# Kernel optimization log

Measured on AMD Instinct MI355X. Metric: run time of the kernel, lower is better.

The kernel has to match this reference:

```python
import jax, jax.numpy as jnp
import numpy as np

B, T, IN, H, NL = 64, 256, 64, 768, 2
LU, OUT = 256, 1
INPUT_SCALE = 1.5
OUTPUT_SCALE = 70.0
STD = 0.001  # nn.init.normal_(p, std=0.001) on all LSTM params


def setup_inputs() -> dict:
    key = jax.random.key(0)
    ks = jax.random.split(key, 16)
    inp = {"x": jax.random.normal(ks[0], (B, T, IN), jnp.float32)}
    dims = [IN, H]
    for l in range(NL):
        d = dims[l]
        inp[f"Wih{l}"] = (jax.random.normal(ks[1 + 4 * l], (4 * H, d)) * STD).astype(jnp.float32)
        inp[f"Whh{l}"] = (jax.random.normal(ks[2 + 4 * l], (4 * H, H)) * STD).astype(jnp.float32)
        inp[f"bih{l}"] = (jax.random.normal(ks[3 + 4 * l], (4 * H,)) * STD).astype(jnp.float32)
        inp[f"bhh{l}"] = (jax.random.normal(ks[4 + 4 * l], (4 * H,)) * STD).astype(jnp.float32)
    # MLP head (torch default-ish small init)
    inp["W1"] = (jax.random.normal(ks[9], (LU, H)) * (1.0 / np.sqrt(H))).astype(jnp.float32)
    inp["b1"] = jnp.zeros((LU,), jnp.float32)
    inp["W2"] = (jax.random.normal(ks[10], (OUT, LU)) * (1.0 / np.sqrt(LU))).astype(jnp.float32)
    inp["b2"] = jnp.zeros((OUT,), jnp.float32)
    return inp


def _lstm_layer(x, Wih, Whh, bih, bhh):
    # x: (B, T, D) -> hidden sequence (B, T, H). PyTorch gate order: i, f, g, o.
    b = x.shape[0]
    h = Whh.shape[1]
    # precompute input contributions for all timesteps: (B, T, 4H)
    xg = jnp.einsum('btd,gd->btg', x, Wih) + bih + bhh

    def step(carry, xt):
        hp, cp = carry
        gates = xt + hp @ Whh.T  # (B, 4H)
        i, f, g, o = jnp.split(gates, 4, axis=-1)
        c = jax.nn.sigmoid(f) * cp + jax.nn.sigmoid(i) * jnp.tanh(g)
        hn = jax.nn.sigmoid(o) * jnp.tanh(c)
        return (hn, c), hn

    h0 = jnp.zeros((b, h), x.dtype)
    (_, _), hs = jax.lax.scan(step, (h0, h0), xg.transpose(1, 0, 2))
    return hs.transpose(1, 0, 2)  # (B, T, H)


def reference(x, Wih0, Whh0, bih0, bhh0, Wih1, Whh1, bih1, bhh1, W1, b1, W2, b2):
    xs = x / INPUT_SCALE
    h1 = _lstm_layer(xs, Wih0, Whh0, bih0, bhh0)
    h2 = _lstm_layer(h1, Wih1, Whh1, bih1, bhh1)
    last = h2[:, -1, :]                       # (B, H)
    z = jax.nn.soft_sign(last @ W1.T + b1)    # Softsign: x / (1 + |x|)
    pred = (z @ W2.T + b2) * OUTPUT_SCALE     # (B, OUT)
    return pred[:, None, :]                   # unsqueeze(1) -> (B, 1, OUT)
```

## Files before the change

kernel.cpp:

```cpp
#include <hip/hip_runtime.h>
#include <hip/hip_bf16.h>


#define B_  64
#define T_  256
#define IN_ 64
#define H_  768
#define G_  3072
#define K0_ 832
#define K1_ 1536
#define NWG0 96
#define NWGC 192
#define NWGT 256
#define CB_  96
#define SLOT_ (CB_ * 64 * 8)

typedef __bf16 bf16_t;
typedef bf16_t bf16x8 __attribute__((ext_vector_type(8)));
typedef float  f32x4  __attribute__((ext_vector_type(4)));

__device__ __forceinline__ unsigned short f2bf(float f) {
    union { float f; unsigned u; } v; v.f = f;
    unsigned r = v.u + 0x7FFFu + ((v.u >> 16) & 1u);
    return (unsigned short)(r >> 16);
}
__device__ __forceinline__ float fast_sigm(float x) {
    float e = __builtin_amdgcn_exp2f(-1.44269504f * x);
    return __builtin_amdgcn_rcpf(1.0f + e);
}
__device__ __forceinline__ float fast_tanh(float x) {
    float e = __builtin_amdgcn_exp2f(2.88539008f * x);
    return (e - 1.0f) * __builtin_amdgcn_rcpf(e + 1.0f);
}
__device__ __forceinline__ void st_llc_u32(unsigned* p, unsigned v) {
    asm volatile("global_store_dword %0, %1, off sc1" :: "v"(p), "v"(v) : "memory");
}
#define MFMA16(a, b, c) __builtin_amdgcn_mfma_f32_16x16x32_bf16((a), (b), (c), 0, 0, 0)
#define AGENT_LD(p) __hip_atomic_load((p), __ATOMIC_RELAXED, __HIP_MEMORY_SCOPE_AGENT)


__global__ __launch_bounds__(256) void prep_kernel(
    const float* __restrict__ x,
    const float* __restrict__ Wih0, const float* __restrict__ Whh0,
    const float* __restrict__ bih0, const float* __restrict__ bhh0,
    const float* __restrict__ Wih1, const float* __restrict__ Whh1,
    const float* __restrict__ bih1, const float* __restrict__ bhh1,
    unsigned short* __restrict__ xsT,
    unsigned short* __restrict__ W0cat,
    unsigned short* __restrict__ W1cat,
    float* __restrict__ bias0, float* __restrict__ bias1,
    int* __restrict__ ctrs)
{
    int i = blockIdx.x * blockDim.x + threadIdx.x;
    int stride = gridDim.x * blockDim.x;
    for (int j = i; j < B_ * T_ * IN_; j += stride) {
        int b = j >> 14;
        int t = (j >> 6) & (T_ - 1);
        int k = j & (IN_ - 1);
        xsT[(((size_t)t * B_) + b) * IN_ + k] = f2bf(x[j] * (1.0f / 1.5f));
    }
    for (int j = i; j < G_ * IN_; j += stride) {
        int r = j >> 6; int k = j & 63;
        W0cat[(size_t)r * K0_ + k] = f2bf(Wih0[j]);
    }
    for (int j = i; j < G_ * H_; j += stride) {
        int r = j / H_; int k = j - r * H_;
        W0cat[(size_t)r * K0_ + IN_ + k] = f2bf(Whh0[j]);
        W1cat[(size_t)r * K1_ + k]       = f2bf(Wih1[j]);
        W1cat[(size_t)r * K1_ + H_ + k]  = f2bf(Whh1[j]);
    }
    for (int j = i; j < G_; j += stride) {
        bias0[j] = bih0[j] + bhh0[j];
        bias1[j] = bih1[j] + bhh1[j];
    }
    for (int j = i; j < 2048; j += stride) ctrs[j] = 0;
}

__global__ __launch_bounds__(256) void lstm_persistent(
    const unsigned short* __restrict__ xsT,
    const unsigned short* __restrict__ W0cat,
    const unsigned short* __restrict__ W1cat,
    const float* __restrict__ bias0, const float* __restrict__ bias1,
    unsigned short* __restrict__ h1ring,
    unsigned short* __restrict__ h2ring,
    float* __restrict__ hf32,
    int* __restrict__ ctrs)
{
    __shared__ unsigned short ldsb[4][16][8];

    const int tid  = threadIdx.x;
    const int lane = tid & 63;
    const int wave = tid >> 6;
    const int wg   = blockIdx.x;

    int* flags0 = &ctrs[0];
    int* flags1 = &ctrs[256];
    int* ep0    = &ctrs[512];
    int* ep1    = &ctrs[768];
    int* done   = &ctrs[1536];

    if (wg == NWGC || wg == NWGC + 1) {
        if (wave != 0) return;
        const bool agg1 = (wg == NWGC + 1);
        int* fl = agg1 ? flags1 : flags0;
        int* ep = agg1 ? ep1 : ep0;
        const int i1 = lane;
        const int i2 = 64 + (lane & 31);
        for (int e = 1; e <= T_; ++e) {
            for (;;) {
                int fa = AGENT_LD(&fl[i1]);
                int fb = AGENT_LD(&fl[i2]);
                if (__all(fa >= e && fb >= e)) break;
                __builtin_amdgcn_s_sleep(1);
            }
            if (lane < 8) st_llc_u32((unsigned*)&ep[lane * 16], (unsigned)e);
        }
        if (agg1 && lane == 0) st_llc_u32((unsigned*)done, 1u);
        return;
    }
    if (wg > NWGC + 1) {
        float a = 1.0f + (float)tid * 1e-7f;
        const float bm = 1.0000001f, cm = 1e-9f;
        for (;;) {
            for (int i = 0; i < 2048; i++)
                a = __builtin_fmaf(a, bm, cm);
            asm volatile("" : "+v"(a));
            int d = 0;
            if (lane == 0) d = AGENT_LD(done);
            d = __builtin_amdgcn_readfirstlane(d);
            if (d != 0) break;
        }
        return;
    }

    const bool isL1 = (wg >= NWG0);
    const int cb   = isL1 ? (wg - NWG0) : wg;
    const int c0   = cb * 8;
    const int frow = lane & 15;
    const int q    = lane >> 4;
    const int kof  = q * 8;
    const int m0   = wave * 16;

    int* myrep0 = &ep0[(wg & 7) * 16];
    int* myrep1 = &ep1[(wg & 7) * 16];

    const unsigned short* Wc = isL1 ? W1cat : W0cat;
    const int Kc = isL1 ? K1_ : K0_;
    int q0 = frow >> 3, col0 = c0 + (frow & 7);
    const unsigned short* Bp0 = Wc + (size_t)(q0 * H_ + col0) * Kc + kof;
    const unsigned short* Bp1 = Wc + (size_t)((2 + q0) * H_ + col0) * Kc + kof;

    const float* bias = isL1 ? bias1 : bias0;
    const bool lowhalf = (lane & 15) < 8;
    const int ecol = c0 + (lane & 7);
    float bi = 0.f, bff = 0.f, bg = 0.f, bo = 0.f;
    if (lowhalf) {
        bi  = bias[0 * H_ + ecol];
        bff = bias[1 * H_ + ecol];
        bg  = bias[2 * H_ + ecol];
        bo  = bias[3 * H_ + ecol];
    }
    float creg[4] = {0.f, 0.f, 0.f, 0.f};

    const size_t aoff = (size_t)q * 512 + (size_t)(m0 + frow) * 8;
    const size_t stoff_e = (size_t)cb * 512 + (size_t)(m0 + (lane >> 2)) * 8
                         + (size_t)(lane & 3) * 2;

    if (!isL1) {
        for (int s = 0; s < T_; ++s) {
            f32x4 acc0 = {0.f, 0.f, 0.f, 0.f};
            f32x4 acc1 = {0.f, 0.f, 0.f, 0.f};
            {
                const unsigned short* xsp =
                    xsT + ((size_t)s * B_ + m0 + frow) * IN_ + kof;
                #pragma unroll
                for (int ki = 0; ki < 2; ki++) {
                    bf16x8 a  = *(const bf16x8*)(xsp + ki * 32);
                    bf16x8 b0 = *(const bf16x8*)(Bp0 + ki * 32);
                    bf16x8 b1 = *(const bf16x8*)(Bp1 + ki * 32);
                    acc0 = MFMA16(a, b0, acc0);
                    acc1 = MFMA16(a, b1, acc1);
                }
            }
            if (s > 0) {
                if (tid == 0) {
                    while (AGENT_LD(myrep0) < s)
                        __builtin_amdgcn_s_sleep(1);
                }
                __syncthreads();
                const unsigned short* hr = h1ring + (size_t)(s - 1) * SLOT_ + aoff;
                #pragma unroll
                for (int kj = 0; kj < 24; kj++) {
                    bf16x8 a  = *(const bf16x8*)(hr + kj * 2048);
                    bf16x8 b0 = *(const bf16x8*)(Bp0 + (kj + 2) * 32);
                    bf16x8 b1 = *(const bf16x8*)(Bp1 + (kj + 2) * 32);
                    acc0 = MFMA16(a, b0, acc0);
                    acc1 = MFMA16(a, b1, acc1);
                }
            }
            f32x4 pacc0, pacc1;
            #pragma unroll
            for (int j = 0; j < 4; j++) {
                pacc0[j] = __shfl_xor(acc0[j], 8);
                pacc1[j] = __shfl_xor(acc1[j], 8);
            }
            if (lowhalf) {
                #pragma unroll
                for (int j = 0; j < 4; j++) {
                    float pi = acc0[j]  + bi;
                    float pf = pacc0[j] + bff;
                    float pg = acc1[j]  + bg;
                    float po = pacc1[j] + bo;
                    float cn = fast_sigm(pf) * creg[j] + fast_sigm(pi) * fast_tanh(pg);
                    float hn = fast_sigm(po) * fast_tanh(cn);
                    creg[j] = cn;
                    ldsb[wave][q * 4 + j][lane & 7] = f2bf(hn);
                }
            }
            unsigned v = ((const unsigned*)&ldsb[wave][0][0])[lane];
            st_llc_u32((unsigned*)(h1ring + (size_t)s * SLOT_ + stoff_e), v);
            __syncthreads();
            if (tid == 0) st_llc_u32((unsigned*)&flags0[cb], (unsigned)(s + 1));
        }
    } else {
        for (int s = 1; s <= T_; ++s) {
            const int t = s - 1;
            if (tid == 0) {
                while (AGENT_LD(myrep0) < s)
                    __builtin_amdgcn_s_sleep(1);
            }
            if (tid == 64 && t > 0) {
                while (AGENT_LD(myrep1) < t)
                    __builtin_amdgcn_s_sleep(1);
            }
            __syncthreads();
            f32x4 acc0 = {0.f, 0.f, 0.f, 0.f};
            f32x4 acc1 = {0.f, 0.f, 0.f, 0.f};
            const unsigned short* h1r = h1ring + (size_t)t * SLOT_ + aoff;
            #pragma unroll
            for (int ki = 0; ki < 24; ki++) {
                bf16x8 a  = *(const bf16x8*)(h1r + ki * 2048);
                bf16x8 b0 = *(const bf16x8*)(Bp0 + ki * 32);
                bf16x8 b1 = *(const bf16x8*)(Bp1 + ki * 32);
                acc0 = MFMA16(a, b0, acc0);
                acc1 = MFMA16(a, b1, acc1);
            }
            if (t > 0) {
                const unsigned short* h2r = h2ring + (size_t)(t - 1) * SLOT_ + aoff;
                #pragma unroll
                for (int ki = 0; ki < 24; ki++) {
                    bf16x8 a  = *(const bf16x8*)(h2r + ki * 2048);
                    bf16x8 b0 = *(const bf16x8*)(Bp0 + (ki + 24) * 32);
                    bf16x8 b1 = *(const bf16x8*)(Bp1 + (ki + 24) * 32);
                    acc0 = MFMA16(a, b0, acc0);
                    acc1 = MFMA16(a, b1, acc1);
                }
            }
            f32x4 pacc0, pacc1;
            #pragma unroll
            for (int j = 0; j < 4; j++) {
                pacc0[j] = __shfl_xor(acc0[j], 8);
                pacc1[j] = __shfl_xor(acc1[j], 8);
            }
            if (lowhalf) {
                #pragma unroll
                for (int j = 0; j < 4; j++) {
                    int row = m0 + q * 4 + j;
                    float pi = acc0[j]  + bi;
                    float pf = pacc0[j] + bff;
                    float pg = acc1[j]  + bg;
                    float po = pacc1[j] + bo;
                    float cn = fast_sigm(pf) * creg[j] + fast_sigm(pi) * fast_tanh(pg);
                    float hn = fast_sigm(po) * fast_tanh(cn);
                    creg[j] = cn;
                    ldsb[wave][q * 4 + j][lane & 7] = f2bf(hn);
                    if (t == T_ - 1) hf32[(size_t)row * H_ + ecol] = hn;
                }
            }
            unsigned v = ((const unsigned*)&ldsb[wave][0][0])[lane];
            st_llc_u32((unsigned*)(h2ring + (size_t)t * SLOT_ + stoff_e), v);
            __syncthreads();
            if (tid == 0) st_llc_u32((unsigned*)&flags1[cb], (unsigned)s);
        }
    }
}

__global__ __launch_bounds__(256) void head_kernel(
    const float* __restrict__ hlast,
    const float* __restrict__ W1, const float* __restrict__ b1,
    const float* __restrict__ W2, const float* __restrict__ b2,
    float* __restrict__ out)
{
    __shared__ float hs[H_];
    __shared__ float partial[4];
    int b = blockIdx.x;
    int tid = threadIdx.x;
    for (int j = tid; j < H_; j += 256) hs[j] = hlast[(size_t)b * H_ + j];
    __syncthreads();
    float z = 0.f;
    const float* w = W1 + (size_t)tid * H_;
    for (int j = 0; j < H_; j++) z += hs[j] * w[j];
    z += b1[tid];
    z = z / (1.0f + fabsf(z));
    float p = z * W2[tid];
    #pragma unroll
    for (int off = 32; off > 0; off >>= 1) p += __shfl_down(p, off, 64);
    if ((tid & 63) == 0) partial[tid >> 6] = p;
    __syncthreads();
    if (tid == 0) {
        float s = partial[0] + partial[1] + partial[2] + partial[3];
        out[b] = (s + b2[0]) * 70.0f;
    }
}

extern "C" void kernel_launch(void* const* d_in, const int* in_sizes, int n_in,
                              void* d_out, int out_size, void* d_ws, size_t ws_size,
                              hipStream_t stream) {
    const float* x    = (const float*)d_in[0];
    const float* Wih0 = (const float*)d_in[1];
    const float* Whh0 = (const float*)d_in[2];
    const float* bih0 = (const float*)d_in[3];
    const float* bhh0 = (const float*)d_in[4];
    const float* Wih1 = (const float*)d_in[5];
    const float* Whh1 = (const float*)d_in[6];
    const float* bih1 = (const float*)d_in[7];
    const float* bhh1 = (const float*)d_in[8];
    const float* W1   = (const float*)d_in[9];
    const float* b1   = (const float*)d_in[10];
    const float* W2   = (const float*)d_in[11];
    const float* b2   = (const float*)d_in[12];
    float* out = (float*)d_out;

    char* w = (char*)d_ws;
    int* ctrs = (int*)w;                          w += 8192;
    unsigned short* h1ring = (unsigned short*)w;  w += (size_t)T_ * SLOT_ * 2;
    unsigned short* h2ring = (unsigned short*)w;  w += (size_t)T_ * SLOT_ * 2;
    unsigned short* xsT    = (unsigned short*)w;  w += (size_t)B_ * T_ * IN_ * 2;
    unsigned short* W0cat  = (unsigned short*)w;  w += (size_t)G_ * K0_ * 2;
    unsigned short* W1cat  = (unsigned short*)w;  w += (size_t)G_ * K1_ * 2;
    float* bias0 = (float*)w;                     w += G_ * 4;
    float* bias1 = (float*)w;                     w += G_ * 4;
    float* hf32  = (float*)w;                     w += (size_t)B_ * H_ * 4;

    prep_kernel<<<1024, 256, 0, stream>>>(x, Wih0, Whh0, bih0, bhh0,
                                          Wih1, Whh1, bih1, bhh1,
                                          xsT, W0cat, W1cat, bias0, bias1, ctrs);
    lstm_persistent<<<NWGT, 256, 0, stream>>>(xsT, W0cat, W1cat, bias0, bias1,
                                              h1ring, h2ring, hf32, ctrs);
    head_kernel<<<B_, 256, 0, stream>>>(hf32, W1, b1, W2, b2, out);
}
```

Measured before the change: 3.166 ms.

## Replace workgroup barriers with per-wave flags and per-wave aggregator epochs

Each wave of a recurrent workgroup now publishes its own completion flag and polls its own epoch counter, removing the __syncthreads barriers around the per-step h handoff. The aggregator workgroups use all four waves, one per wave-slice of flags. The counter region is enlarged to hold these. The spinning filler workgroups now run eight independent FMA chains instead of one. The aim is to cut intra-workgroup barrier latency on the serial timestep critical path, at the cost of more polling traffic and more flag writes.

```diff
diff --git a/kernel.cpp b/kernel.cpp
--- a/kernel.cpp
+++ b/kernel.cpp
@@ -38,6 +38,16 @@
 #define MFMA16(a, b, c) __builtin_amdgcn_mfma_f32_16x16x32_bf16((a), (b), (c), 0, 0, 0)
 #define AGENT_LD(p) __hip_atomic_load((p), __ATOMIC_RELAXED, __HIP_MEMORY_SCOPE_AGENT)
 
+__device__ __forceinline__ void wait_ep(int* rep, int s, int lane) {
+    for (;;) {
+        int e = 0;
+        if (lane == 0) e = AGENT_LD(rep);
+        e = __builtin_amdgcn_readfirstlane(e);
+        if (e >= s) break;
+        __builtin_amdgcn_s_sleep(1);
+    }
+    asm volatile("" ::: "memory");
+}
 
 __global__ __launch_bounds__(256) void prep_kernel(
     const float* __restrict__ x,
@@ -73,7 +83,7 @@
         bias0[j] = bih0[j] + bhh0[j];
         bias1[j] = bih1[j] + bhh1[j];
     }
-    for (int j = i; j < 2048; j += stride) ctrs[j] = 0;
+    for (int j = i; j < 4096; j += stride) ctrs[j] = 0;
 }
 
 __global__ __launch_bounds__(256) void lstm_persistent(
@@ -93,17 +103,12 @@
     const int wave = tid >> 6;
     const int wg   = blockIdx.x;
 
-    int* flags0 = &ctrs[0];
-    int* flags1 = &ctrs[256];
-    int* ep0    = &ctrs[512];
-    int* ep1    = &ctrs[768];
-    int* done   = &ctrs[1536];
+    int* done = &ctrs[2048];
 
     if (wg == NWGC || wg == NWGC + 1) {
-        if (wave != 0) return;
-        const bool agg1 = (wg == NWGC + 1);
-        int* fl = agg1 ? flags1 : flags0;
-        int* ep = agg1 ? ep1 : ep0;
+        const int layer = wg - NWGC;
+        int* fl = &ctrs[layer * 512 + wave * 128];
+        int* ep = &ctrs[1024 + layer * 512 + wave * 128];
         const int i1 = lane;
         const int i2 = 64 + (lane & 31);
         for (int e = 1; e <= T_; ++e) {
@@ -115,16 +120,24 @@
             }
             if (lane < 8) st_llc_u32((unsigned*)&ep[lane * 16], (unsigned)e);
         }
-        if (agg1 && lane == 0) st_llc_u32((unsigned*)done, 1u);
+        if (layer == 1 && wave == 3 && lane == 0)
+            st_llc_u32((unsigned*)done, 1u);
         return;
     }
     if (wg > NWGC + 1) {
-        float a = 1.0f + (float)tid * 1e-7f;
+        float a0 = 1.0f, a1 = 1.1f, a2 = 1.2f, a3 = 1.3f;
+        float a4 = 1.4f, a5 = 1.5f, a6 = 1.6f, a7 = 1.7f;
         const float bm = 1.0000001f, cm = 1e-9f;
         for (;;) {
-            for (int i = 0; i < 2048; i++)
-                a = __builtin_fmaf(a, bm, cm);
-            asm volatile("" : "+v"(a));
+            #pragma unroll
+            for (int i = 0; i < 256; i++) {
+                a0 = __builtin_fmaf(a0, bm, cm); a1 = __builtin_fmaf(a1, bm, cm);
+                a2 = __builtin_fmaf(a2, bm, cm); a3 = __builtin_fmaf(a3, bm, cm);
+                a4 = __builtin_fmaf(a4, bm, cm); a5 = __builtin_fmaf(a5, bm, cm);
+                a6 = __builtin_fmaf(a6, bm, cm); a7 = __builtin_fmaf(a7, bm, cm);
+            }
+            asm volatile("" : "+v"(a0), "+v"(a1), "+v"(a2), "+v"(a3),
+                              "+v"(a4), "+v"(a5), "+v"(a6), "+v"(a7));
             int d = 0;
             if (lane == 0) d = AGENT_LD(done);
             d = __builtin_amdgcn_readfirstlane(d);
@@ -141,8 +154,9 @@
     const int kof  = q * 8;
     const int m0   = wave * 16;
 
-    int* myrep0 = &ep0[(wg & 7) * 16];
-    int* myrep1 = &ep1[(wg & 7) * 16];
+    int* myflag = &ctrs[(isL1 ? 512 : 0) + wave * 128 + cb];
+    int* rep0   = &ctrs[1024 + wave * 128 + (wg & 7) * 16];
+    int* rep1   = &ctrs[1536 + wave * 128 + (wg & 7) * 16];
 
     const unsigned short* Wc = isL1 ? W1cat : W0cat;
     const int Kc = isL1 ? K1_ : K0_;
@@ -183,11 +197,7 @@
                 }
             }
             if (s > 0) {
-                if (tid == 0) {
-                    while (AGENT_LD(myrep0) < s)
-                        __builtin_amdgcn_s_sleep(1);
-                }
-                __syncthreads();
+                wait_ep(rep0, s, lane);
                 const unsigned short* hr = h1ring + (size_t)(s - 1) * SLOT_ + aoff;
                 #pragma unroll
                 for (int kj = 0; kj < 24; kj++) {
@@ -219,21 +229,14 @@
             }
             unsigned v = ((const unsigned*)&ldsb[wave][0][0])[lane];
             st_llc_u32((unsigned*)(h1ring + (size_t)s * SLOT_ + stoff_e), v);
-            __syncthreads();
-            if (tid == 0) st_llc_u32((unsigned*)&flags0[cb], (unsigned)(s + 1));
+            asm volatile("s_waitcnt vmcnt(0)" ::: "memory");
+            if (lane == 0) st_llc_u32((unsigned*)myflag, (unsigned)(s + 1));
         }
     } else {
         for (int s = 1; s <= T_; ++s) {
             const int t = s - 1;
-            if (tid == 0) {
-                while (AGENT_LD(myrep0) < s)
-                    __builtin_amdgcn_s_sleep(1);
-            }
-            if (tid == 64 && t > 0) {
-                while (AGENT_LD(myrep1) < t)
-                    __builtin_amdgcn_s_sleep(1);
-            }
-            __syncthreads();
+            wait_ep(rep0, s, lane);
+            if (t > 0) wait_ep(rep1, t, lane);
             f32x4 acc0 = {0.f, 0.f, 0.f, 0.f};
             f32x4 acc1 = {0.f, 0.f, 0.f, 0.f};
             const unsigned short* h1r = h1ring + (size_t)t * SLOT_ + aoff;
@@ -279,8 +282,8 @@
             }
             unsigned v = ((const unsigned*)&ldsb[wave][0][0])[lane];
             st_llc_u32((unsigned*)(h2ring + (size_t)t * SLOT_ + stoff_e), v);
-            __syncthreads();
-            if (tid == 0) st_llc_u32((unsigned*)&flags1[cb], (unsigned)s);
+            asm volatile("s_waitcnt vmcnt(0)" ::: "memory");
+            if (lane == 0) st_llc_u32((unsigned*)myflag, (unsigned)s);
         }
     }
 }
@@ -332,7 +335,7 @@
     float* out = (float*)d_out;
 
     char* w = (char*)d_ws;
-    int* ctrs = (int*)w;                          w += 8192;
+    int* ctrs = (int*)w;                          w += 16384;
     unsigned short* h1ring = (unsigned short*)w;  w += (size_t)T_ * SLOT_ * 2;
     unsigned short* h2ring = (unsigned short*)w;  w += (size_t)T_ * SLOT_ * 2;
     unsigned short* xsT    = (unsigned short*)w;  w += (size_t)B_ * T_ * IN_ * 2;
```

Result: slower. 4.469 ms (+41.2%).
